# Kernel optimization log

Hardware: AMD Instinct MI355X
Metric: run time of the kernel (lower is better)

## Reference

```python
import jax, jax.numpy as jnp
import numpy as np

HID = 768
NH = 12
HD = HID // NH
EPS = 1e-12


def _layernorm(x, g, b):
    m = x.mean(-1, keepdims=True)
    v = ((x - m) ** 2).mean(-1, keepdims=True)
    return (x - m) / jnp.sqrt(v + EPS) * g + b


def _mha_block(x, mask, Wq, bq, Wk, bk, Wv, bv, Wo, bo, ln_g, ln_b):
    # x: [B,S,H]; mask broadcastable to [B,NH,S,S] (additive)
    B, S, _ = x.shape
    split = lambda t: t.reshape(B, S, NH, HD).transpose(0, 2, 1, 3)  # [B,NH,S,HD]
    q = split(x @ Wq + bq)
    k = split(x @ Wk + bk)
    v = split(x @ Wv + bv)
    scores = jnp.einsum('bhqd,bhkd->bhqk', q, k) / np.float32(np.sqrt(HD)) + mask
    probs = jax.nn.softmax(scores, axis=-1)
    ctx = jnp.einsum('bhqk,bhkd->bhqd', probs, v)
    ctx = ctx.transpose(0, 2, 1, 3).reshape(B, S, HID)
    # BertSelfOutput: dense + residual + LayerNorm
    return _layernorm(ctx @ Wo + bo + x, ln_g, ln_b)


def setup_inputs() -> dict:
    key = jax.random.key(0)
    ks = jax.random.split(key, 32)
    B, S = 32, 512
    scale = 0.02
    W = lambda i, di, do: jax.random.normal(ks[i], (di, do), jnp.float32) * scale
    inp = {
        'hidden_states': jax.random.normal(ks[0], (B, S, HID), jnp.float32),
        'attention_mask': jnp.zeros((B, 1, 1, S), jnp.float32),
        # token-level attention params
        'Wq': W(1, HID, HID), 'bq': jnp.zeros((HID,), jnp.float32),
        'Wk': W(2, HID, HID), 'bk': jnp.zeros((HID,), jnp.float32),
        'Wv': W(3, HID, HID), 'bv': jnp.zeros((HID,), jnp.float32),
        'Wao': W(4, HID, HID), 'bao': jnp.zeros((HID,), jnp.float32),
        'ln1_g': jnp.ones((HID,), jnp.float32), 'ln1_b': jnp.zeros((HID,), jnp.float32),
        # dialog (CLS-level) attention params
        'dWq': W(5, HID, HID), 'dbq': jnp.zeros((HID,), jnp.float32),
        'dWk': W(6, HID, HID), 'dbk': jnp.zeros((HID,), jnp.float32),
        'dWv': W(7, HID, HID), 'dbv': jnp.zeros((HID,), jnp.float32),
        'dWo': W(8, HID, HID), 'dbo': jnp.zeros((HID,), jnp.float32),
        'dln_g': jnp.ones((HID,), jnp.float32), 'dln_b': jnp.zeros((HID,), jnp.float32),
        # FFN params
        'Wi': W(9, HID, 4 * HID), 'bi': jnp.zeros((4 * HID,), jnp.float32),
        'Wo2': W(10, 4 * HID, HID), 'bo2': jnp.zeros((HID,), jnp.float32),
        'ln2_g': jnp.ones((HID,), jnp.float32), 'ln2_b': jnp.zeros((HID,), jnp.float32),
        'turns': 8,
    }
    return inp


def reference(hidden_states, attention_mask,
              Wq, bq, Wk, bk, Wv, bv, Wao, bao, ln1_g, ln1_b,
              dWq, dbq, dWk, dbk, dWv, dbv, dWo, dbo, dln_g, dln_b,
              Wi, bi, Wo2, bo2, ln2_g, ln2_b, turns):
    # 1) token-level self-attention + SelfOutput
    x = _mha_block(hidden_states, attention_mask,
                   Wq, bq, Wk, bk, Wv, bv, Wao, bao, ln1_g, ln1_b)
    # 2) hierarchical dialog attention over per-turn CLS tokens
    bs = x.shape[0] // turns
    cls = x[:, 0].reshape(bs, turns, HID)
    pos = jnp.arange(turns)
    # faithful to source: (j >= i) -> -10000 (masks diagonal and future)
    cmask = (pos[None, :] >= pos[:, None]).astype(x.dtype) * (-10000.0)
    cmask = cmask[None, None, :, :]  # broadcast to [bs, NH, turns, turns]
    cls = _mha_block(cls, cmask, dWq, dbq, dWk, dbk, dWv, dbv, dWo, dbo, dln_g, dln_b)
    x = x.at[:, 0].set(cls.reshape(-1, HID))
    # 3) FFN: intermediate (gelu) + output dense + residual + LayerNorm
    inter = jax.nn.gelu(x @ Wi + bi, approximate=False)
    out = _layernorm(inter @ Wo2 + bo2 + x, ln2_g, ln2_b)
    return out
```

## Files before the change

kernel.cpp:

```cpp
#include <hip/hip_runtime.h>
#include <hip/hip_bf16.h>
#include <math.h>

using bf16 = __hip_bfloat16;
typedef __attribute__((ext_vector_type(8))) __bf16 bf16x8;
typedef __attribute__((ext_vector_type(4))) __bf16 bf16x4;
typedef __attribute__((ext_vector_type(4))) float f32x4;
typedef __attribute__((ext_vector_type(16))) float f32x16;
typedef unsigned int u32x2 __attribute__((ext_vector_type(2)));

__device__ __forceinline__ float b2f(bf16 x){ return __bfloat162float(x); }
__device__ __forceinline__ bf16  f2b(float x){ return __float2bfloat16(x); }
__device__ __forceinline__ float ldf(const float* p, size_t i){ return p[i]; }
__device__ __forceinline__ float ldf(const bf16*  p, size_t i){ return b2f(p[i]); }
__device__ __forceinline__ void stf(float* p, size_t i, float v){ p[i] = v; }
__device__ __forceinline__ void stf(bf16*  p, size_t i, float v){ p[i] = f2b(v); }

__device__ __forceinline__ void st4(float* p, float a, float b, float c, float d){
  float4 f; f.x=a; f.y=b; f.z=c; f.w=d; *(float4*)p = f;
}
__device__ __forceinline__ void st4(bf16* p, float a, float b, float c, float d){
  bf16x4 o; o[0]=(__bf16)a; o[1]=(__bf16)b; o[2]=(__bf16)c; o[3]=(__bf16)d;
  *(bf16x4*)p = o;
}

__device__ __forceinline__ float gelu_f(float v){
  float u = v*(0.7978845608f + 0.0356774081f*v*v);
  float e = __expf(2.f*u);
  float t = 1.f - 2.f/(e+1.f);
  return 0.5f*v*(1.f+t);
}

typedef const __attribute__((address_space(1))) unsigned int* gas_u32p;
typedef __attribute__((address_space(3))) unsigned int* las_u32p;
__device__ __forceinline__ void gl_lds16(const bf16* g, bf16* l){
  __builtin_amdgcn_global_load_lds((gas_u32p)(const void*)g, (las_u32p)(void*)l, 16, 0, 0);
}

#define MFMA16 __builtin_amdgcn_mfma_f32_16x16x32_bf16
#define MFMA32 __builtin_amdgcn_mfma_f32_32x32x16_bf16

#define LGKM(N) do { \
  asm volatile("s_waitcnt lgkmcnt(" #N ")" ::: "memory"); \
  __builtin_amdgcn_sched_barrier(0); \
} while(0)

__device__ __forceinline__ unsigned cvtpk(float lo, float hi){
  unsigned w;
  asm("v_cvt_pk_bf16_f32 %0, %1, %2" : "=v"(w) : "v"(lo), "v"(hi));
  return w;
}
__device__ __forceinline__ void plswap(unsigned &a, unsigned &b){
  u32x2 r = __builtin_amdgcn_permlane32_swap(a, b, false, false);
  a = r[0]; b = r[1];
}

#define NHEAD 12
#define HDIM  64
#define HID   768
#define SEQ   512
#define BATCH 32
#define ROWS  (BATCH*SEQ)
#define QKVW  2304
#define QCH   128
#define NCHUNK (SEQ/QCH)
#define FT    128

template<int EPI, typename TR>
__global__ __launch_bounds__(512,2)
void gemm8p(const bf16* __restrict__ A, int lda,
            const bf16* __restrict__ Bt, int ldb,
            bf16* __restrict__ C, int ldc, int K,
            const float* __restrict__ bias,
            const TR* __restrict__ res, int ldres)
{
  __shared__ __align__(16) bf16 tileLds[4][256*64];

  const int tid  = threadIdx.x;
  const int wave = tid>>6, lane = tid&63;
  const int r = lane&15, qd = lane>>4;
  const int wr = wave>>2, wc = wave&3;
  const int m0 = blockIdx.y*256, n0 = blockIdx.x*256;
  const int NTK = K>>6;
  const int wbase = wave*512;

  const int sr = tid>>3, sp = tid&7;
  const bf16* pA = A  + (size_t)(m0+sr)*lda + ((sp^(sr&7))<<3);
  const bf16* pB = Bt + (size_t)(n0+sr)*ldb + ((sp^(sr&7))<<3);

  auto stage = [&](int H){
    const int u = H>>2, idx = H&3, bufi = u&1;
    const size_t kof = (size_t)u*64;
    if (idx==0){
      gl_lds16(pA + kof,                    tileLds[bufi*2] + wbase);
      gl_lds16(pA + kof + (size_t)64*lda,   tileLds[bufi*2] + wbase + 4096);
    } else if (idx==3){
      gl_lds16(pA + kof + (size_t)128*lda,  tileLds[bufi*2] + 8192 + wbase);
      gl_lds16(pA + kof + (size_t)192*lda,  tileLds[bufi*2] + 8192 + wbase + 4096);
    } else {
      const int h = idx-1;
      gl_lds16(pB + kof + (size_t)(h*128)*ldb,
               tileLds[bufi*2+1] + h*8192 + wbase);
      gl_lds16(pB + kof + (size_t)(h*128+64)*ldb,
               tileLds[bufi*2+1] + h*8192 + wbase + 4096);
    }
  };

  auto rdA = [&](const bf16* base, int mi, int ks)->bf16x8{
    const int row = mi*32 + wr*16 + r;
    return *(const bf16x8*)(base + row*64 + ((((ks<<2)|qd) ^ (r&7))<<3));
  };
  auto rdB = [&](const bf16* base, int nj, int ks)->bf16x8{
    const int row = nj*64 + wc*16 + r;
    return *(const bf16x8*)(base + row*64 + ((((ks<<2)|qd) ^ (r&7))<<3));
  };

  #pragma unroll
  for (int H=0; H<7; ++H) stage(H);
  asm volatile("s_waitcnt vmcnt(6)" ::: "memory");
  __builtin_amdgcn_s_barrier();

  f32x4 acc[8][4] = {};

  for (int t=0; t<NTK; ++t){
    const bf16* a = tileLds[(t&1)*2];
    const bf16* b = tileLds[(t&1)*2+1];
    const int Hb = 4*t + 6;
    const int Hmax = 4*NTK;
    bf16x8 af[4][2], bn0[2][2], bn1[2][2];

    af[0][0]=rdA(a,0,0); af[0][1]=rdA(a,0,1);
    af[1][0]=rdA(a,1,0); af[1][1]=rdA(a,1,1);
    bn0[0][0]=rdB(b,0,0); bn0[0][1]=rdB(b,0,1);
    bn0[1][0]=rdB(b,1,0); bn0[1][1]=rdB(b,1,1);
    __builtin_amdgcn_sched_barrier(0);
    af[2][0]=rdA(a,2,0); af[2][1]=rdA(a,2,1);
    af[3][0]=rdA(a,3,0); af[3][1]=rdA(a,3,1);
    if (Hb+1 < Hmax) stage(Hb+1);
    LGKM(4);
    __builtin_amdgcn_s_setprio(1);
    #pragma unroll
    for (int mi=0;mi<2;mi++)
      #pragma unroll
      for (int nj=0;nj<2;nj++){
        acc[mi][nj] = MFMA16(af[mi][0], bn0[nj][0], acc[mi][nj],0,0,0);
        acc[mi][nj] = MFMA16(af[mi][1], bn0[nj][1], acc[mi][nj],0,0,0);
      }
    LGKM(0);
    #pragma unroll
    for (int mi=2;mi<4;mi++)
      #pragma unroll
      for (int nj=0;nj<2;nj++){
        acc[mi][nj] = MFMA16(af[mi][0], bn0[nj][0], acc[mi][nj],0,0,0);
        acc[mi][nj] = MFMA16(af[mi][1], bn0[nj][1], acc[mi][nj],0,0,0);
      }
    __builtin_amdgcn_s_setprio(0);
    __builtin_amdgcn_s_barrier();

    bn1[0][0]=rdB(b,2,0); bn1[0][1]=rdB(b,2,1);
    __builtin_amdgcn_sched_barrier(0);
    bn1[1][0]=rdB(b,3,0); bn1[1][1]=rdB(b,3,1);
    if (Hb+2 < Hmax) stage(Hb+2);
    LGKM(2);
    __builtin_amdgcn_s_setprio(1);
    #pragma unroll
    for (int mi=0;mi<4;mi++){
      acc[mi][2] = MFMA16(af[mi][0], bn1[0][0], acc[mi][2],0,0,0);
      acc[mi][2] = MFMA16(af[mi][1], bn1[0][1], acc[mi][2],0,0,0);
    }
    LGKM(0);
    #pragma unroll
    for (int mi=0;mi<4;mi++){
      acc[mi][3] = MFMA16(af[mi][0], bn1[1][0], acc[mi][3],0,0,0);
      acc[mi][3] = MFMA16(af[mi][1], bn1[1][1], acc[mi][3],0,0,0);
    }
    __builtin_amdgcn_s_setprio(0);
    __builtin_amdgcn_s_barrier();

    af[0][0]=rdA(a,4,0); af[0][1]=rdA(a,4,1);
    af[1][0]=rdA(a,5,0); af[1][1]=rdA(a,5,1);
    __builtin_amdgcn_sched_barrier(0);
    af[2][0]=rdA(a,6,0); af[2][1]=rdA(a,6,1);
    af[3][0]=rdA(a,7,0); af[3][1]=rdA(a,7,1);
    if (Hb+3 < Hmax) stage(Hb+3);
    LGKM(4);
    __builtin_amdgcn_s_setprio(1);
    #pragma unroll
    for (int mi=0;mi<2;mi++)
      #pragma unroll
      for (int nj=0;nj<2;nj++){
        acc[4+mi][2+nj] = MFMA16(af[mi][0], bn1[nj][0], acc[4+mi][2+nj],0,0,0);
        acc[4+mi][2+nj] = MFMA16(af[mi][1], bn1[nj][1], acc[4+mi][2+nj],0,0,0);
      }
    LGKM(0);
    #pragma unroll
    for (int mi=2;mi<4;mi++)
      #pragma unroll
      for (int nj=0;nj<2;nj++){
        acc[4+mi][2+nj] = MFMA16(af[mi][0], bn1[nj][0], acc[4+mi][2+nj],0,0,0);
        acc[4+mi][2+nj] = MFMA16(af[mi][1], bn1[nj][1], acc[4+mi][2+nj],0,0,0);
      }
    __builtin_amdgcn_s_setprio(0);
    __builtin_amdgcn_s_barrier();

    if (Hb+4 < Hmax) stage(Hb+4);
    __builtin_amdgcn_s_setprio(1);
    #pragma unroll
    for (int mi=0;mi<4;mi++)
      #pragma unroll
      for (int nj=0;nj<2;nj++){
        acc[4+mi][nj] = MFMA16(af[mi][0], bn0[nj][0], acc[4+mi][nj],0,0,0);
        acc[4+mi][nj] = MFMA16(af[mi][1], bn0[nj][1], acc[4+mi][nj],0,0,0);
      }
    __builtin_amdgcn_s_setprio(0);
    if (t < NTK-2) { asm volatile("s_waitcnt vmcnt(6)" ::: "memory"); }
    else           { asm volatile("s_waitcnt vmcnt(0)" ::: "memory"); }
    __builtin_amdgcn_s_barrier();
  }

  float bs[4];
  #pragma unroll
  for (int nj=0;nj<4;nj++)
    bs[nj] = bias ? bias[n0 + nj*64 + wc*16 + r] : 0.f;
  #pragma unroll
  for (int mi=0;mi<8;mi++){
    #pragma unroll
    for (int nj=0;nj<4;nj++){
      #pragma unroll
      for (int i=0;i<4;i++){
        const int mm = m0 + mi*32 + wr*16 + qd*4 + i;
        const int nn = n0 + nj*64 + wc*16 + r;
        float v = acc[mi][nj][i] + bs[nj];
        if (EPI==1) v = gelu_f(v);
        if (EPI==2) v += ldf(res, (size_t)mm*ldres + nn);
        C[(size_t)mm*ldc + nn] = f2b(v);
      }
    }
  }
}

__global__ __launch_bounds__(256)
void flash_attn(const bf16* __restrict__ qkv, const bf16* __restrict__ vtb,
                const float* __restrict__ mask, bf16* __restrict__ ctx)
{
  const int qc = blockIdx.x;
  const int z  = blockIdx.y;
  const int b  = z / NHEAD, h = z - b*NHEAD;
  const int q0 = qc*QCH;

  __shared__ __align__(16) bf16 Ks[FT*64];
  __shared__ __align__(16) bf16 Vts[64*FT];
  __shared__ __align__(16) float smask[FT];

  const int tid = threadIdx.x;
  const int wave = tid>>6, lane = tid&63;
  const int l31 = lane&31, hi = lane>>5;
  const int wr = wave;

  const bf16* Qg = qkv + ((size_t)(b*SEQ + q0))*QKVW + h*HDIM;
  const bf16* Kg = qkv + ((size_t)b*SEQ)*QKVW + 768 + h*HDIM;
  const bf16* Vg = vtb + (size_t)z*HDIM*SEQ;

  auto stageK = [&](int k0){
    #pragma unroll
    for (int c0=0;c0<1024;c0+=256){
      int c = c0+tid, row = c>>3, pos = c&7;
      gl_lds16(Kg + (size_t)(k0+row)*QKVW + ((pos^(row&7))*8),
               Ks + (size_t)(c0 + wave*64)*8);
    }
  };
  auto stageV = [&](int k0){
    #pragma unroll
    for (int c0=0;c0<1024;c0+=256){
      int c = c0+tid, row = c>>4, pos = c&15;
      gl_lds16(Vg + (size_t)row*SEQ + k0 + ((pos^(row&7))*8),
               Vts + (size_t)(c0 + wave*64)*8);
    }
  };

  stageK(0);
  stageV(0);
  if (tid < FT) smask[tid] = 8.0f*mask[(size_t)b*SEQ + tid];
  bf16x8 qf[4];
  #pragma unroll
  for (int hs=0;hs<4;hs++)
    qf[hs] = *(const bf16x8*)(Qg + (size_t)(wr*32+l31)*QKVW + hs*16 + hi*8);

  f32x16 accO[2] = {};
  float mrun = -1e30f, lrun = 0.f;

  for (int k0=0; k0<SEQ; k0+=FT){
    __syncthreads();

    f32x16 S[4];
    #pragma unroll
    for (int kb=0;kb<4;kb++){
      #pragma unroll
      for (int rq=0;rq<4;rq++){
        f32x4 mq = *(const f32x4*)(smask + kb*32 + rq*8 + hi*4);
        S[kb][rq*4+0]=mq[0]; S[kb][rq*4+1]=mq[1];
        S[kb][rq*4+2]=mq[2]; S[kb][rq*4+3]=mq[3];
      }
    }
    #pragma unroll
    for (int hs=0;hs<4;hs++){
      bf16x8 kf[4];
      #pragma unroll
      for (int kb=0;kb<4;kb++){
        int row = kb*32 + l31;
        int ch  = hs*2 + hi;
        kf[kb] = *(const bf16x8*)(Ks + row*64 + ((ch^(row&7))*8));
      }
      #pragma unroll
      for (int kb=0;kb<4;kb++)
        S[kb] = MFMA32(kf[kb], qf[hs], S[kb], 0,0,0);
    }

    __syncthreads();
    if (k0+FT < SEQ) stageK(k0+FT);

    float mx = -1e30f;
    #pragma unroll
    for (int kb=0;kb<4;kb++)
      #pragma unroll
      for (int e=0;e<16;e++){
        float v = S[kb][e]*0.125f;
        S[kb][e] = v;
        mx = fmaxf(mx, v);
      }
    mx = fmaxf(mx, __shfl_xor(mx, 32));
    float mnew = fmaxf(mrun, mx);
    float alpha = __expf(mrun - mnew);
    mrun = mnew;
    float ps = 0.f;
    #pragma unroll
    for (int kb=0;kb<4;kb++)
      #pragma unroll
      for (int e=0;e<16;e++){
        float p = __expf(S[kb][e] - mnew);
        S[kb][e] = p;
        ps += p;
      }
    ps += __shfl_xor(ps, 32);
    lrun = lrun*alpha + ps;
    #pragma unroll
    for (int dt=0;dt<2;dt++)
      #pragma unroll
      for (int e=0;e<16;e++)
        accO[dt][e] *= alpha;

    #pragma unroll
    for (int kb=0;kb<4;kb++){
      unsigned w[8];
      #pragma unroll
      for (int m=0;m<8;m++)
        w[m] = cvtpk(S[kb][2*m], S[kb][2*m+1]);
      plswap(w[0], w[2]);  plswap(w[1], w[3]);
      plswap(w[4], w[6]);  plswap(w[5], w[7]);
      union { unsigned u[4]; bf16x8 v; } pf0, pf1;
      pf0.u[0]=w[0]; pf0.u[1]=w[1]; pf0.u[2]=w[2]; pf0.u[3]=w[3];
      pf1.u[0]=w[4]; pf1.u[1]=w[5]; pf1.u[2]=w[6]; pf1.u[3]=w[7];
      #pragma unroll
      for (int ks2=0;ks2<2;ks2++){
        const bf16x8 pf = ks2 ? pf1.v : pf0.v;
        #pragma unroll
        for (int dt=0;dt<2;dt++){
          int row = dt*32 + l31;
          int ch  = kb*4 + ks2*2 + hi;
          bf16x8 vf = *(const bf16x8*)(Vts + row*FT + ((ch^(row&7))*8));
          accO[dt] = MFMA32(vf, pf, accO[dt], 0,0,0);
        }
      }
    }

    __syncthreads();
    if (k0+FT < SEQ){
      stageV(k0+FT);
      if (tid < FT) smask[tid] = 8.0f*mask[(size_t)b*SEQ + k0+FT + tid];
    }
  }

  float invl = 1.0f/lrun;
  bf16* Cg = ctx + ((size_t)(b*SEQ + q0 + wr*32 + l31))*HID + h*HDIM;
  #pragma unroll
  for (int dt=0;dt<2;dt++){
    #pragma unroll
    for (int rq=0;rq<4;rq++){
      union { unsigned long long u; __bf16 hh[4]; } pk;
      #pragma unroll
      for (int i=0;i<4;i++)
        pk.hh[i] = (__bf16)(accO[dt][rq*4+i]*invl);
      *(unsigned long long*)(Cg + dt*32 + rq*8 + hi*4) = pk.u;
    }
  }
}

__global__ void transpose_cast(const float* __restrict__ in, bf16* __restrict__ out,
                               int R, int C)
{
  __shared__ float tile[32][33];
  int bc = blockIdx.x*32, br = blockIdx.y*32;
  int tx = threadIdx.x, ty = threadIdx.y;
  #pragma unroll
  for (int i=ty;i<32;i+=8)
    tile[i][tx] = in[(size_t)(br+i)*C + bc+tx];
  __syncthreads();
  #pragma unroll
  for (int i=ty;i<32;i+=8)
    out[(size_t)(bc+i)*R + br+tx] = f2b(tile[tx][i]);
}

__global__ void transpose_cast4(const float* __restrict__ w0, const float* __restrict__ w1,
                                const float* __restrict__ w2, const float* __restrict__ w3,
                                bf16* __restrict__ out)
{
  const float* in = blockIdx.z==0?w0 : blockIdx.z==1?w1 : blockIdx.z==2?w2 : w3;
  bf16* o = out + (size_t)blockIdx.z*768*768;
  __shared__ float tile[32][33];
  int bc = blockIdx.x*32, br = blockIdx.y*32;
  int tx = threadIdx.x, ty = threadIdx.y;
  #pragma unroll
  for (int i=ty;i<32;i+=8)
    tile[i][tx] = in[(size_t)(br+i)*768 + bc+tx];
  __syncthreads();
  #pragma unroll
  for (int i=ty;i<32;i+=8)
    o[(size_t)(bc+i)*768 + br+tx] = f2b(tile[tx][i]);
}

__global__ __launch_bounds__(256)
void castX(const float* __restrict__ in, bf16* __restrict__ out)
{
  int i = blockIdx.x*256 + threadIdx.x;
  float4 f = ((const float4*)in)[i];
  union{ unsigned long long u; __bf16 h[4]; } pk;
  pk.h[0]=(__bf16)f.x; pk.h[1]=(__bf16)f.y; pk.h[2]=(__bf16)f.z; pk.h[3]=(__bf16)f.w;
  ((unsigned long long*)out)[i] = pk.u;
}

__global__ void concat_bias(const float* __restrict__ a, const float* __restrict__ b,
                            const float* __restrict__ c, float* __restrict__ o)
{
  int i = blockIdx.x*256 + threadIdx.x;
  if (i < 768) o[i] = a[i];
  else if (i < 1536) o[i] = b[i-768];
  else if (i < 2304) o[i] = c[i-1536];
}

__global__ void vtrans(const bf16* __restrict__ v, bf16* __restrict__ vt)
{
  int z = blockIdx.z; int b = z/NHEAD, h = z - b*NHEAD;
  int d0 = blockIdx.x*32, s0 = blockIdx.y*32;
  __shared__ bf16 t[32][33];
  int tx = threadIdx.x, ty = threadIdx.y;
  #pragma unroll
  for (int i=ty;i<32;i+=8)
    t[i][tx] = v[(size_t)(b*SEQ + s0+i)*QKVW + h*HDIM + d0+tx];
  __syncthreads();
  #pragma unroll
  for (int i=ty;i<32;i+=8)
    vt[(size_t)z*HDIM*SEQ + (size_t)(d0+i)*SEQ + s0+tx] = t[tx][i];
}

template<typename TO>
__global__ __launch_bounds__(256)
void ln768(const bf16* __restrict__ y, const float* __restrict__ g,
           const float* __restrict__ be, TO* __restrict__ dst)
{
  const int wave = threadIdx.x>>6, lane = threadIdx.x&63;
  const size_t row = (size_t)blockIdx.x*4 + wave;
  const bf16* yr = y + row*HID;
  float x[12];
  float s = 0.f, q = 0.f;
  #pragma unroll
  for (int c=0;c<3;c++){
    bf16x4 v = *(const bf16x4*)(yr + c*256 + lane*4);
    #pragma unroll
    for (int j=0;j<4;j++){
      float f = (float)v[j];
      x[c*4+j] = f;
      s += f; q += f*f;
    }
  }
  #pragma unroll
  for (int off=1; off<64; off<<=1){ s += __shfl_xor(s, off); q += __shfl_xor(q, off); }
  float mean = s*(1.0f/HID);
  float var  = q*(1.0f/HID) - mean*mean;
  float inv  = rsqrtf(var + 1e-12f);
  TO* dr = dst + row*HID;
  #pragma unroll
  for (int c=0;c<3;c++){
    float4 gg = *(const float4*)(g  + c*256 + lane*4);
    float4 bb = *(const float4*)(be + c*256 + lane*4);
    st4(dr + c*256 + lane*4,
        (x[c*4+0]-mean)*inv*gg.x + bb.x,
        (x[c*4+1]-mean)*inv*gg.y + bb.y,
        (x[c*4+2]-mean)*inv*gg.z + bb.z,
        (x[c*4+3]-mean)*inv*gg.w + bb.w);
  }
}

__global__ __launch_bounds__(256)
void cls_proj(const bf16* __restrict__ x2,
              const float* __restrict__ Wq, const float* __restrict__ bq,
              const float* __restrict__ Wk, const float* __restrict__ bk,
              const float* __restrict__ Wv, const float* __restrict__ bv,
              bf16* __restrict__ oq, bf16* __restrict__ ok, bf16* __restrict__ ov)
{
  int mat = blockIdx.x, row = blockIdx.y;
  const float* W  = mat==0 ? Wq : (mat==1 ? Wk : Wv);
  const float* bi = mat==0 ? bq : (mat==1 ? bk : bv);
  bf16* out       = mat==0 ? oq : (mat==1 ? ok : ov);
  __shared__ float a[HID];
  const bf16* xr = x2 + (size_t)row*SEQ*HID;
  for (int i=threadIdx.x;i<HID;i+=256) a[i] = b2f(xr[i]);
  __syncthreads();
  for (int c0=0;c0<HID;c0+=256){
    int col = c0 + threadIdx.x;
    float acc = 0.f;
    for (int k=0;k<HID;k++) acc += a[k]*W[(size_t)k*HID + col];
    out[(size_t)row*HID + col] = f2b(acc + bi[col]);
  }
}

__global__ __launch_bounds__(64)
void cls_attn(const bf16* __restrict__ q, const bf16* __restrict__ k,
              const bf16* __restrict__ v, bf16* __restrict__ ctx)
{
  int z = blockIdx.x; int bb = z/NHEAD, h = z - bb*NHEAD;
  __shared__ float P[8][8];
  int t = threadIdx.x;
  int qi = t>>3, ki = t&7;
  float s = 0.f;
  for (int d=0; d<HDIM; d++)
    s += b2f(q[(size_t)(bb*8+qi)*HID + h*HDIM + d]) *
         b2f(k[(size_t)(bb*8+ki)*HID + h*HDIM + d]);
  s = s*0.125f + (ki >= qi ? -10000.0f : 0.0f);
  float m = s;
  #pragma unroll
  for (int off=4; off; off>>=1) m = fmaxf(m, __shfl_xor(m, off, 8));
  float e = __expf(s - m);
  float sum = e;
  #pragma unroll
  for (int off=4; off; off>>=1) sum += __shfl_xor(sum, off, 8);
  P[qi][ki] = e/sum;
  __syncthreads();
  for (int q2=0; q2<8; q2++){
    float acc = 0.f;
    #pragma unroll
    for (int k2=0; k2<8; k2++)
      acc += P[q2][k2] * b2f(v[(size_t)(bb*8+k2)*HID + h*HDIM + t]);
    ctx[(size_t)(bb*8+q2)*HID + h*HDIM + t] = f2b(acc);
  }
}

__global__ __launch_bounds__(256)
void cls_out(const bf16* __restrict__ ctx, const float* __restrict__ Wo,
             const float* __restrict__ bo, const float* __restrict__ g,
             const float* __restrict__ be, bf16* __restrict__ x2)
{
  int row = blockIdx.x;
  __shared__ float a[HID];
  __shared__ float yrow[HID];
  const bf16* cr = ctx + (size_t)row*HID;
  bf16* xr = x2 + (size_t)row*SEQ*HID;
  for (int i=threadIdx.x;i<HID;i+=256) a[i] = b2f(cr[i]);
  __syncthreads();
  for (int c0=0;c0<HID;c0+=256){
    int col = c0 + threadIdx.x;
    float acc = 0.f;
    for (int k=0;k<HID;k++) acc += a[k]*Wo[(size_t)k*HID + col];
    yrow[col] = acc + bo[col] + b2f(xr[col]);
  }
  __syncthreads();
  int t = threadIdx.x;
  float x0 = yrow[t], x1 = yrow[t+256], x2v = yrow[t+512];
  float s = x0+x1+x2v, qq = x0*x0+x1*x1+x2v*x2v;
  #pragma unroll
  for (int off=32; off; off>>=1){ s += __shfl_xor(s, off); qq += __shfl_xor(qq, off); }
  __shared__ float rs[4], rq[4];
  int wv = t>>6;
  if ((t&63)==0){ rs[wv]=s; rq[wv]=qq; }
  __syncthreads();
  s = rs[0]+rs[1]+rs[2]+rs[3];
  qq = rq[0]+rq[1]+rq[2]+rq[3];
  float mean = s*(1.0f/HID);
  float var  = qq*(1.0f/HID) - mean*mean;
  float inv  = rsqrtf(var + 1e-12f);
  xr[t    ] = f2b((x0 -mean)*inv*g[t    ] + be[t    ]);
  xr[t+256] = f2b((x1 -mean)*inv*g[t+256] + be[t+256]);
  xr[t+512] = f2b((x2v-mean)*inv*g[t+512] + be[t+512]);
}

extern "C" void kernel_launch(void* const* d_in, const int* in_sizes, int n_in,
                              void* d_out, int out_size, void* d_ws, size_t ws_size,
                              hipStream_t stream)
{
  const float* X    = (const float*)d_in[0];
  const float* AM   = (const float*)d_in[1];
  const float* Wq   = (const float*)d_in[2];  const float* bq  = (const float*)d_in[3];
  const float* Wk   = (const float*)d_in[4];  const float* bk  = (const float*)d_in[5];
  const float* Wv   = (const float*)d_in[6];  const float* bv  = (const float*)d_in[7];
  const float* Wao  = (const float*)d_in[8];  const float* bao = (const float*)d_in[9];
  const float* ln1g = (const float*)d_in[10]; const float* ln1b= (const float*)d_in[11];
  const float* dWq  = (const float*)d_in[12]; const float* dbq = (const float*)d_in[13];
  const float* dWk  = (const float*)d_in[14]; const float* dbk = (const float*)d_in[15];
  const float* dWv  = (const float*)d_in[16]; const float* dbv = (const float*)d_in[17];
  const float* dWo  = (const float*)d_in[18]; const float* dbo = (const float*)d_in[19];
  const float* dlng = (const float*)d_in[20]; const float* dlnb= (const float*)d_in[21];
  const float* Wi   = (const float*)d_in[22]; const float* bi  = (const float*)d_in[23];
  const float* Wo2  = (const float*)d_in[24]; const float* bo2 = (const float*)d_in[25];
  const float* ln2g = (const float*)d_in[26]; const float* ln2b= (const float*)d_in[27];
  float* OUT = (float*)d_out;

  char* wp = (char*)d_ws;
  auto alloc = [&](size_t elems)->bf16*{
    bf16* p = (bf16*)wp;
    wp += ((elems*sizeof(bf16) + 255)/256)*256;
    return p;
  };
  bf16* wtq  = alloc(768*768);
  bf16* wtk  = alloc(768*768);
  bf16* wtv  = alloc(768*768);
  bf16* wtao = alloc(768*768);
  bf16* wti  = alloc((size_t)768*3072);
  bf16* wto2 = alloc((size_t)3072*768);
  float* bqkv = (float*)alloc(2304*2);
  bf16* qkv  = alloc((size_t)ROWS*QKVW);
  bf16* vtb  = alloc((size_t)ROWS*HID);
  bf16* inter = qkv;
  bf16* scb  = alloc((size_t)ROWS*HID);
  bf16* yb   = scb;
  bf16* x2   = scb;
  bf16* ctxb = alloc((size_t)ROWS*HID);
  bf16* xb   = ctxb;
  bf16* clsq = alloc(32*HID);
  bf16* clsk = alloc(32*HID);
  bf16* clsv = alloc(32*HID);
  bf16* clsc = alloc(32*HID);
  (void)wtk; (void)wtv;

  dim3 T32(32,8);
  transpose_cast4<<<dim3(24,24,4), T32, 0, stream>>>(Wq, Wk, Wv, Wao, wtq);
  transpose_cast<<<dim3(96,24), T32, 0, stream>>>(Wi,  wti, 768, 3072);
  transpose_cast<<<dim3(24,96), T32, 0, stream>>>(Wo2, wto2,3072, 768);
  concat_bias<<<9,256,0,stream>>>(bq, bk, bv, bqkv);
  castX<<<ROWS*HID/4/256,256,0,stream>>>(X, xb);

  gemm8p<0,float><<<dim3(9,64),512,0,stream>>>(
      xb,768,  wtq,768,  qkv,QKVW, 768, bqkv, (const float*)nullptr, 0);

  vtrans<<<dim3(2,16,BATCH*NHEAD), T32, 0, stream>>>(qkv + 1536, vtb);

  flash_attn<<<dim3(NCHUNK, BATCH*NHEAD),256,0,stream>>>(qkv, vtb, AM, ctxb);

  gemm8p<2,float><<<dim3(3,64),512,0,stream>>>(
      ctxb,768,  wtao,768,  yb,768, 768, bao, X, 768);
  ln768<bf16><<<ROWS/4,256,0,stream>>>(yb, ln1g, ln1b, x2);

  cls_proj<<<dim3(3,32),256,0,stream>>>(x2, dWq,dbq, dWk,dbk, dWv,dbv,
                                        clsq, clsk, clsv);
  cls_attn<<<48,64,0,stream>>>(clsq, clsk, clsv, clsc);
  cls_out<<<32,256,0,stream>>>(clsc, dWo, dbo, dlng, dlnb, x2);

  gemm8p<1,float><<<dim3(12,64),512,0,stream>>>(
      x2,768,  wti,768,  inter,3072, 768, bi, (const float*)nullptr, 0);
  gemm8p<2,bf16><<<dim3(3,64),512,0,stream>>>(
      inter,3072,  wto2,3072,  yb,768, 3072, bo2, x2, 768);
  ln768<float><<<ROWS/4,256,0,stream>>>(yb, ln2g, ln2b, OUT);
}
```

Measured before the change: 813.1 us.

## Restructure GEMM main loop into whole-tile staging with register-prefetched A fragments

Replaces the four quarter-tile global-to-LDS stages per iteration with a single stage call that loads both the A and B tiles for the next K step. It also cuts the per-iteration barriers from four to one. The A fragments for the next tile are read into registers right after the barrier, so the last MFMA group overlaps those LDS reads. The cost is a shallower pipeline: each iteration waits with vmcnt(0) for the next tile, so global latency must hide behind one iteration of compute. The prologue also loads tile 1 a second time, which is redundant.

```diff
diff --git a/kernel.cpp b/kernel.cpp
--- a/kernel.cpp
+++ b/kernel.cpp
@@ -88,22 +88,19 @@
   const bf16* pA = A  + (size_t)(m0+sr)*lda + ((sp^(sr&7))<<3);
   const bf16* pB = Bt + (size_t)(n0+sr)*ldb + ((sp^(sr&7))<<3);
 
-  auto stage = [&](int H){
-    const int u = H>>2, idx = H&3, bufi = u&1;
-    const size_t kof = (size_t)u*64;
-    if (idx==0){
-      gl_lds16(pA + kof,                    tileLds[bufi*2] + wbase);
-      gl_lds16(pA + kof + (size_t)64*lda,   tileLds[bufi*2] + wbase + 4096);
-    } else if (idx==3){
-      gl_lds16(pA + kof + (size_t)128*lda,  tileLds[bufi*2] + 8192 + wbase);
-      gl_lds16(pA + kof + (size_t)192*lda,  tileLds[bufi*2] + 8192 + wbase + 4096);
-    } else {
-      const int h = idx-1;
-      gl_lds16(pB + kof + (size_t)(h*128)*ldb,
-               tileLds[bufi*2+1] + h*8192 + wbase);
-      gl_lds16(pB + kof + (size_t)(h*128+64)*ldb,
-               tileLds[bufi*2+1] + h*8192 + wbase + 4096);
-    }
+  auto stageAll = [&](int t){
+    const int bufi = t&1;
+    const size_t kof = (size_t)t*64;
+    bf16* la = tileLds[bufi*2]   + wbase;
+    bf16* lb = tileLds[bufi*2+1] + wbase;
+    gl_lds16(pA + kof,                   la);
+    gl_lds16(pA + kof + (size_t)64*lda,  la + 4096);
+    gl_lds16(pA + kof + (size_t)128*lda, la + 8192);
+    gl_lds16(pA + kof + (size_t)192*lda, la + 12288);
+    gl_lds16(pB + kof,                   lb);
+    gl_lds16(pB + kof + (size_t)64*ldb,  lb + 4096);
+    gl_lds16(pB + kof + (size_t)128*ldb, lb + 8192);
+    gl_lds16(pB + kof + (size_t)192*ldb, lb + 12288);
   };
 
   auto rdA = [&](const bf16* base, int mi, int ks)->bf16x8{
@@ -115,107 +112,86 @@
     return *(const bf16x8*)(base + row*64 + ((((ks<<2)|qd) ^ (r&7))<<3));
   };
 
-  #pragma unroll
-  for (int H=0; H<7; ++H) stage(H);
-  asm volatile("s_waitcnt vmcnt(6)" ::: "memory");
+  stageAll(0);
+  if (NTK > 1) stageAll(1);
+  asm volatile("s_waitcnt vmcnt(8)" ::: "memory");
   __builtin_amdgcn_s_barrier();
 
   f32x4 acc[8][4] = {};
+  bf16x8 afA[4][2], afB[4][2], bn0[2][2], bn1[2][2];
+
+  {
+    const bf16* a0 = tileLds[0];
+    #pragma unroll
+    for (int mi=0;mi<4;mi++){ afA[mi][0]=rdA(a0,mi,0); afA[mi][1]=rdA(a0,mi,1); }
+    __builtin_amdgcn_sched_barrier(0);
+  }
 
   for (int t=0; t<NTK; ++t){
     const bf16* a = tileLds[(t&1)*2];
     const bf16* b = tileLds[(t&1)*2+1];
-    const int Hb = 4*t + 6;
-    const int Hmax = 4*NTK;
-    bf16x8 af[4][2], bn0[2][2], bn1[2][2];
-
-    af[0][0]=rdA(a,0,0); af[0][1]=rdA(a,0,1);
-    af[1][0]=rdA(a,1,0); af[1][1]=rdA(a,1,1);
+
     bn0[0][0]=rdB(b,0,0); bn0[0][1]=rdB(b,0,1);
     bn0[1][0]=rdB(b,1,0); bn0[1][1]=rdB(b,1,1);
     __builtin_amdgcn_sched_barrier(0);
-    af[2][0]=rdA(a,2,0); af[2][1]=rdA(a,2,1);
-    af[3][0]=rdA(a,3,0); af[3][1]=rdA(a,3,1);
-    if (Hb+1 < Hmax) stage(Hb+1);
+    bn1[0][0]=rdB(b,2,0); bn1[0][1]=rdB(b,2,1);
+    bn1[1][0]=rdB(b,3,0); bn1[1][1]=rdB(b,3,1);
+    if (t+2 <= NTK-1+1 && t+1 < NTK) stageAll(t+1);
+
     LGKM(4);
     __builtin_amdgcn_s_setprio(1);
     #pragma unroll
-    for (int mi=0;mi<2;mi++)
+    for (int mi=0;mi<4;mi++)
       #pragma unroll
       for (int nj=0;nj<2;nj++){
-        acc[mi][nj] = MFMA16(af[mi][0], bn0[nj][0], acc[mi][nj],0,0,0);
-        acc[mi][nj] = MFMA16(af[mi][1], bn0[nj][1], acc[mi][nj],0,0,0);
-      }
+        acc[mi][nj] = MFMA16(afA[mi][0], bn0[nj][0], acc[mi][nj],0,0,0);
+        acc[mi][nj] = MFMA16(afA[mi][1], bn0[nj][1], acc[mi][nj],0,0,0);
+      }
+    __builtin_amdgcn_s_setprio(0);
+
+    #pragma unroll
+    for (int mi=0;mi<4;mi++){ afB[mi][0]=rdA(a,4+mi,0); afB[mi][1]=rdA(a,4+mi,1); }
+    LGKM(8);
+    __builtin_amdgcn_s_setprio(1);
+    #pragma unroll
+    for (int mi=0;mi<4;mi++)
+      #pragma unroll
+      for (int nj=0;nj<2;nj++){
+        acc[mi][2+nj] = MFMA16(afA[mi][0], bn1[nj][0], acc[mi][2+nj],0,0,0);
+        acc[mi][2+nj] = MFMA16(afA[mi][1], bn1[nj][1], acc[mi][2+nj],0,0,0);
+      }
+    __builtin_amdgcn_s_setprio(0);
+
     LGKM(0);
-    #pragma unroll
-    for (int mi=2;mi<4;mi++)
+    __builtin_amdgcn_s_setprio(1);
+    #pragma unroll
+    for (int mi=0;mi<4;mi++)
       #pragma unroll
       for (int nj=0;nj<2;nj++){
-        acc[mi][nj] = MFMA16(af[mi][0], bn0[nj][0], acc[mi][nj],0,0,0);
-        acc[mi][nj] = MFMA16(af[mi][1], bn0[nj][1], acc[mi][nj],0,0,0);
+        acc[4+mi][2+nj] = MFMA16(afB[mi][0], bn1[nj][0], acc[4+mi][2+nj],0,0,0);
+        acc[4+mi][2+nj] = MFMA16(afB[mi][1], bn1[nj][1], acc[4+mi][2+nj],0,0,0);
       }
     __builtin_amdgcn_s_setprio(0);
+
+    asm volatile("s_waitcnt vmcnt(0)" ::: "memory");
     __builtin_amdgcn_s_barrier();
 
-    bn1[0][0]=rdB(b,2,0); bn1[0][1]=rdB(b,2,1);
-    __builtin_amdgcn_sched_barrier(0);
-    bn1[1][0]=rdB(b,3,0); bn1[1][1]=rdB(b,3,1);
-    if (Hb+2 < Hmax) stage(Hb+2);
-    LGKM(2);
+    if (t+1 < NTK){
+      const bf16* an = tileLds[((t+1)&1)*2];
+      #pragma unroll
+      for (int mi=0;mi<4;mi++){ afA[mi][0]=rdA(an,mi,0); afA[mi][1]=rdA(an,mi,1); }
+      __builtin_amdgcn_sched_barrier(0);
+    }
+
     __builtin_amdgcn_s_setprio(1);
     #pragma unroll
-    for (int mi=0;mi<4;mi++){
-      acc[mi][2] = MFMA16(af[mi][0], bn1[0][0], acc[mi][2],0,0,0);
-      acc[mi][2] = MFMA16(af[mi][1], bn1[0][1], acc[mi][2],0,0,0);
-    }
-    LGKM(0);
-    #pragma unroll
-    for (int mi=0;mi<4;mi++){
-      acc[mi][3] = MFMA16(af[mi][0], bn1[1][0], acc[mi][3],0,0,0);
-      acc[mi][3] = MFMA16(af[mi][1], bn1[1][1], acc[mi][3],0,0,0);
-    }
+    for (int mi=0;mi<4;mi++)
+      #pragma unroll
+      for (int nj=0;nj<2;nj++){
+        acc[4+mi][nj] = MFMA16(afB[mi][0], bn0[nj][0], acc[4+mi][nj],0,0,0);
+        acc[4+mi][nj] = MFMA16(afB[mi][1], bn0[nj][1], acc[4+mi][nj],0,0,0);
+      }
     __builtin_amdgcn_s_setprio(0);
-    __builtin_amdgcn_s_barrier();
-
-    af[0][0]=rdA(a,4,0); af[0][1]=rdA(a,4,1);
-    af[1][0]=rdA(a,5,0); af[1][1]=rdA(a,5,1);
-    __builtin_amdgcn_sched_barrier(0);
-    af[2][0]=rdA(a,6,0); af[2][1]=rdA(a,6,1);
-    af[3][0]=rdA(a,7,0); af[3][1]=rdA(a,7,1);
-    if (Hb+3 < Hmax) stage(Hb+3);
-    LGKM(4);
-    __builtin_amdgcn_s_setprio(1);
-    #pragma unroll
-    for (int mi=0;mi<2;mi++)
-      #pragma unroll
-      for (int nj=0;nj<2;nj++){
-        acc[4+mi][2+nj] = MFMA16(af[mi][0], bn1[nj][0], acc[4+mi][2+nj],0,0,0);
-        acc[4+mi][2+nj] = MFMA16(af[mi][1], bn1[nj][1], acc[4+mi][2+nj],0,0,0);
-      }
-    LGKM(0);
-    #pragma unroll
-    for (int mi=2;mi<4;mi++)
-      #pragma unroll
-      for (int nj=0;nj<2;nj++){
-        acc[4+mi][2+nj] = MFMA16(af[mi][0], bn1[nj][0], acc[4+mi][2+nj],0,0,0);
-        acc[4+mi][2+nj] = MFMA16(af[mi][1], bn1[nj][1], acc[4+mi][2+nj],0,0,0);
-      }
-    __builtin_amdgcn_s_setprio(0);
-    __builtin_amdgcn_s_barrier();
-
-    if (Hb+4 < Hmax) stage(Hb+4);
-    __builtin_amdgcn_s_setprio(1);
-    #pragma unroll
-    for (int mi=0;mi<4;mi++)
-      #pragma unroll
-      for (int nj=0;nj<2;nj++){
-        acc[4+mi][nj] = MFMA16(af[mi][0], bn0[nj][0], acc[4+mi][nj],0,0,0);
-        acc[4+mi][nj] = MFMA16(af[mi][1], bn0[nj][1], acc[4+mi][nj],0,0,0);
-      }
-    __builtin_amdgcn_s_setprio(0);
-    if (t < NTK-2) { asm volatile("s_waitcnt vmcnt(6)" ::: "memory"); }
-    else           { asm volatile("s_waitcnt vmcnt(0)" ::: "memory"); }
-    __builtin_amdgcn_s_barrier();
   }
 
   float bs[4];
```

Result: faster. 780.2 us (-4.1%).
